# Performance work log

Hardware: AMD Instinct MI355X
Metric: run time of the kernel (lower is better)

## Reference

```python
import jax, jax.numpy as jnp
import numpy as np

N_NODES = 100000
N_EDGES = 1600000
F = 64
UNITS = 64


def setup_inputs() -> dict:
    key = jax.random.key(0)
    k = jax.random.split(key, 8)
    x = jax.random.normal(k[0], (N_NODES, F), dtype=jnp.float32)
    edge_index = jax.random.randint(k[1], (2, N_EDGES), 0, N_NODES, dtype=jnp.int32)
    edge_weight = jnp.ones((N_EDGES,), dtype=jnp.float32)
    # glorot-uniform-ish params
    def glorot(kk, shape):
        lim = np.sqrt(6.0 / (shape[0] + shape[1]))
        return jax.random.uniform(kk, shape, dtype=jnp.float32, minval=-lim, maxval=lim)
    mlp_kernel = glorot(k[2], (F, UNITS))
    mlp_bias = jnp.zeros((UNITS,), dtype=jnp.float32)
    neighs_kernel = glorot(k[3], (UNITS, UNITS))
    self_kernel = glorot(k[4], (F, UNITS))
    bias = jnp.zeros((2 * UNITS,), dtype=jnp.float32)
    return {"x": x, "edge_index": edge_index, "edge_weight": edge_weight,
            "mlp_kernel": mlp_kernel, "mlp_bias": mlp_bias,
            "neighs_kernel": neighs_kernel, "self_kernel": self_kernel, "bias": bias}


def reference(x, edge_index, edge_weight, mlp_kernel, mlp_bias, neighs_kernel, self_kernel, bias):
    num_nodes = x.shape[0]
    row, col = edge_index[0], edge_index[1]
    # gcn_mapper: neighbor message scaled by edge weight (original forces weights to 1)
    neighbor_x = x[col] * edge_weight[:, None]            # [E, F]
    h = jax.nn.relu(neighbor_x @ mlp_kernel + mlp_bias)   # [E, U]
    # unsorted_segment_mean over destination row (empty segments -> 0, matching TF)
    seg_sum = jax.ops.segment_sum(h, row, num_segments=num_nodes)              # [N, U]
    cnt = jax.ops.segment_sum(jnp.ones_like(row, dtype=h.dtype), row, num_segments=num_nodes)
    reduced_h = seg_sum / jnp.maximum(cnt, 1.0)[:, None]
    from_neighs = reduced_h @ neighs_kernel               # [N, U]
    from_x = x @ self_kernel                              # [N, U]
    out = jnp.concatenate([from_neighs, from_x], axis=1) + bias
    out = jax.nn.relu(out)                                # [N, 2U]
    return out
```

## Files before the change

### kernel.cpp

```cpp
#include <hip/hip_runtime.h>

#define MAXSLICE 12544
#define MAXSUB   800
#define NBH 32
#define IDXCAP 512

static __device__ __forceinline__ float relu_f(float v) { return fmaxf(v, 0.f); }

static __device__ __forceinline__ unsigned short f2bf(float f) {
  unsigned u = __float_as_uint(f);
  u += 0x7fffu + ((u >> 16) & 1u);
  return (unsigned short)(u >> 16);
}
static __device__ __forceinline__ float bf2f(unsigned short h) {
  return __uint_as_float(((unsigned)h) << 16);
}

__global__ __launch_bounds__(256) void k_node_dual_gemm(
    const float* __restrict__ x, const float* __restrict__ mk,
    const float* __restrict__ sk, const float* __restrict__ bias,
    unsigned short* __restrict__ xwh, float* __restrict__ out, int n_nodes,
    int* __restrict__ bcur0)
{
  __shared__ float s_mk[64][64];
  __shared__ float s_sk[64][64];
  __shared__ float s_xT[64][68];
  const int tid = threadIdx.x;
  if (bcur0 && blockIdx.x == 0 && tid < 8) bcur0[tid] = 0;
  for (int i = tid; i < 4096; i += 256) {
    s_mk[i >> 6][i & 63] = mk[i];
    s_sk[i >> 6][i & 63] = sk[i];
  }
  const int node0 = blockIdx.x * 64;
  for (int i = tid; i < 4096; i += 256) {
    int nl = i >> 6, f = i & 63;
    int n = node0 + nl;
    s_xT[f][nl] = (n < n_nodes) ? x[(size_t)n * 64 + f] : 0.f;
  }
  __syncthreads();
  const int g  = tid >> 4;
  const int ub = (tid & 15) * 4;
  float am[4][4] = {{0.f}};
  float as[4][4] = {{0.f}};
  for (int f = 0; f < 64; ++f) {
    float4 wm = *(const float4*)&s_mk[f][ub];
    float4 ws = *(const float4*)&s_sk[f][ub];
    float4 xv = *(const float4*)&s_xT[f][4 * g];
    const float xs[4] = {xv.x, xv.y, xv.z, xv.w};
#pragma unroll
    for (int j = 0; j < 4; ++j) {
      am[j][0] += xs[j] * wm.x; am[j][1] += xs[j] * wm.y;
      am[j][2] += xs[j] * wm.z; am[j][3] += xs[j] * wm.w;
      as[j][0] += xs[j] * ws.x; as[j][1] += xs[j] * ws.y;
      as[j][2] += xs[j] * ws.z; as[j][3] += xs[j] * ws.w;
    }
  }
  float4 bv = *(const float4*)&bias[64 + ub];
#pragma unroll
  for (int j = 0; j < 4; ++j) {
    int n = node0 + 4 * g + j;
    if (n >= n_nodes) break;
    ushort4 o1 = make_ushort4(f2bf(am[j][0]), f2bf(am[j][1]),
                              f2bf(am[j][2]), f2bf(am[j][3]));
    *(ushort4*)&xwh[(size_t)n * 64 + ub] = o1;
    *(float4*)&out[(size_t)n * 128 + 64 + ub] =
        make_float4(relu_f(as[j][0] + bv.x), relu_f(as[j][1] + bv.y),
                    relu_f(as[j][2] + bv.z), relu_f(as[j][3] + bv.w));
  }
}

__global__ __launch_bounds__(256) void k_count(
    const int* __restrict__ row, int* __restrict__ cnt, int n_edges)
{
  int e = blockIdx.x * 256 + threadIdx.x;
  if (e < n_edges) atomicAdd(&cnt[row[e]], 1);
}

__global__ __launch_bounds__(256) void k_build_sliced(
    const int* __restrict__ row, const int* __restrict__ col,
    const float* __restrict__ ew, int* __restrict__ off,
    int2* __restrict__ elist, int n_edges, int n_nodes)
{
  const int slice = blockIdx.x & 7;
  const int vb    = blockIdx.x >> 3;
  const int nvb   = gridDim.x >> 3;
  const int sliceN = (n_nodes + 7) >> 3;
  const int lo = slice * sliceN;
  const int hi = min(lo + sliceN, n_nodes);
  for (int e = vb * 256 + threadIdx.x; e < n_edges; e += nvb * 256) {
    int r = row[e];
    if (r >= lo && r < hi) {
      int pos = atomicAdd(&off[r], 1);
      elist[pos] = make_int2(col[e], __float_as_int(ew[e]));
    }
  }
}

__global__ __launch_bounds__(1024) void k_bsum(
    const int* __restrict__ cnt, int* __restrict__ bsum, int n)
{
  __shared__ int s[1024];
  int tid = threadIdx.x;
  int i = blockIdx.x * 1024 + tid;
  s[tid] = (i < n) ? cnt[i] : 0;
  __syncthreads();
  for (int d = 512; d > 0; d >>= 1) {
    if (tid < d) s[tid] += s[tid + d];
    __syncthreads();
  }
  if (tid == 0) bsum[blockIdx.x] = s[0];
}

__global__ __launch_bounds__(1024) void k_boffs(
    const int* __restrict__ cnt, const int* __restrict__ bsum,
    int* __restrict__ off, int n, int nb)
{
  __shared__ int s[1024];
  __shared__ int sp[128];
  int tid = threadIdx.x;
  if (tid < 128) {
    int acc = 0;
    for (int j = tid; j < blockIdx.x && j < nb; j += 128) acc += bsum[j];
    sp[tid] = acc;
  }
  int i = blockIdx.x * 1024 + tid;
  int v = (i < n) ? cnt[i] : 0;
  s[tid] = v;
  __syncthreads();
  for (int d = 64; d > 0; d >>= 1) {
    if (tid < d) sp[tid] += sp[tid + d];
    __syncthreads();
  }
  for (int d = 1; d < 1024; d <<= 1) {
    int t = (tid >= d) ? s[tid - d] : 0;
    __syncthreads();
    s[tid] += t;
    __syncthreads();
  }
  if (i < n) off[i] = s[tid] - v + sp[0];
}

__global__ __launch_bounds__(256) void k_bin(
    const int* __restrict__ row, const int* __restrict__ col,
    const float* __restrict__ ew,
    int* __restrict__ brow, int2* __restrict__ bpair,
    int* __restrict__ bcur, int n_edges, int sliceN, int cap)
{
  __shared__ int  s_wcnt[4][8];
  __shared__ int  s_tot[8];
  __shared__ int  s_toff[8];
  __shared__ int  s_gaddr[8];
  __shared__ int  s_rowst[1024];
  __shared__ int2 s_pairst[1024];
  const int tid  = threadIdx.x;
  const int wave = tid >> 6;
  const int lane = tid & 63;
  const unsigned usliceN = (unsigned)sliceN;
  const int stride = gridDim.x * 1024;
  for (int e0 = blockIdx.x * 1024; e0 < n_edges; e0 += stride) {
    const int e = e0 + 4 * tid;
    int   rr[4], cc[4];
    float ww[4];
    int   ss[4];
    if (e + 3 < n_edges) {
      int4 r4   = *(const int4*)&row[e];
      int4 c4   = *(const int4*)&col[e];
      float4 w4 = *(const float4*)&ew[e];
      rr[0] = r4.x; rr[1] = r4.y; rr[2] = r4.z; rr[3] = r4.w;
      cc[0] = c4.x; cc[1] = c4.y; cc[2] = c4.z; cc[3] = c4.w;
      ww[0] = w4.x; ww[1] = w4.y; ww[2] = w4.z; ww[3] = w4.w;
#pragma unroll
      for (int j = 0; j < 4; ++j) ss[j] = (int)((unsigned)rr[j] / usliceN);
    } else {
#pragma unroll
      for (int j = 0; j < 4; ++j) {
        int ej = e + j;
        bool v = ej < n_edges;
        rr[j] = v ? row[ej] : 0;
        cc[j] = v ? col[ej] : 0;
        ww[j] = v ? ew[ej]  : 0.f;
        ss[j] = v ? (int)((unsigned)rr[j] / usliceN) : -1;
      }
    }
#pragma unroll
    for (int b = 0; b < 8; ++b) {
      int c = 0;
#pragma unroll
      for (int j = 0; j < 4; ++j) c += __popcll(__ballot(ss[j] == b));
      if (lane == 0) s_wcnt[wave][b] = c;
    }
    __syncthreads();
    if (wave == 0 && lane < 8) {
      const int b = lane;
      int t0 = s_wcnt[0][b], t1 = s_wcnt[1][b], t2 = s_wcnt[2][b], t3 = s_wcnt[3][b];
      int tot = t0 + t1 + t2 + t3;
      s_tot[b] = tot;
      s_wcnt[0][b] = 0;
      s_wcnt[1][b] = t0;
      s_wcnt[2][b] = t0 + t1;
      s_wcnt[3][b] = t0 + t1 + t2;
      int gbase = tot ? atomicAdd(&bcur[b], tot) : 0;
      int pre = 0;
#pragma unroll
      for (int j2 = 0; j2 < 8; ++j2) pre += (j2 < b) ? s_tot[j2] : 0;
      s_toff[b]  = pre;
      s_gaddr[b] = b * cap + gbase - pre;
    }
    __syncthreads();
#pragma unroll
    for (int b = 0; b < 8; ++b) {
      const int sb = s_toff[b] + s_wcnt[wave][b];
      int off_local = 0;
#pragma unroll
      for (int j = 0; j < 4; ++j) {
        unsigned long long mm = __ballot(ss[j] == b);
        if (ss[j] == b) {
          int rank = __popcll(mm & ((1ull << lane) - 1ull));
          int slot = sb + off_local + rank;
          s_rowst[slot]  = rr[j];
          s_pairst[slot] = make_int2(cc[j], __float_as_int(ww[j]));
        }
        off_local += __popcll(mm);
      }
    }
    __syncthreads();
    const int total = s_toff[7] + s_tot[7];
    for (int i2 = tid; i2 < total; i2 += 256) {
      int b = 0;
#pragma unroll
      for (int j2 = 1; j2 < 8; ++j2) b += (i2 >= s_toff[j2]) ? 1 : 0;
      int a = s_gaddr[b] + i2;
      if (a < (b + 1) * cap) {
        brow[a]  = s_rowst[i2];
        bpair[a] = s_pairst[i2];
      }
    }
    __syncthreads();
  }
}

__global__ __launch_bounds__(256) void k_bin_idx(
    const int* __restrict__ row,
    int* __restrict__ brow, int* __restrict__ bidx,
    int* __restrict__ bcur, int n_edges, int sliceN, int cap)
{
  __shared__ int s_wcnt[4][8];
  __shared__ int s_tot[8];
  __shared__ int s_toff[8];
  __shared__ int s_gaddr[8];
  __shared__ int s_rowst[1024];
  __shared__ int s_idxst[1024];
  const int tid  = threadIdx.x;
  const int wave = tid >> 6;
  const int lane = tid & 63;
  const unsigned usliceN = (unsigned)sliceN;
  const int stride = gridDim.x * 1024;
  for (int e0 = blockIdx.x * 1024; e0 < n_edges; e0 += stride) {
    const int e = e0 + 4 * tid;
    int rr[4], ss[4];
    if (e + 3 < n_edges) {
      int4 r4 = *(const int4*)&row[e];
      rr[0] = r4.x; rr[1] = r4.y; rr[2] = r4.z; rr[3] = r4.w;
#pragma unroll
      for (int j = 0; j < 4; ++j) ss[j] = (int)((unsigned)rr[j] / usliceN);
    } else {
#pragma unroll
      for (int j = 0; j < 4; ++j) {
        int ej = e + j;
        bool v = ej < n_edges;
        rr[j] = v ? row[ej] : 0;
        ss[j] = v ? (int)((unsigned)rr[j] / usliceN) : -1;
      }
    }
#pragma unroll
    for (int b = 0; b < 8; ++b) {
      int c = 0;
#pragma unroll
      for (int j = 0; j < 4; ++j) c += __popcll(__ballot(ss[j] == b));
      if (lane == 0) s_wcnt[wave][b] = c;
    }
    __syncthreads();
    if (wave == 0 && lane < 8) {
      const int b = lane;
      int t0 = s_wcnt[0][b], t1 = s_wcnt[1][b], t2 = s_wcnt[2][b], t3 = s_wcnt[3][b];
      int tot = t0 + t1 + t2 + t3;
      s_tot[b] = tot;
      s_wcnt[0][b] = 0;
      s_wcnt[1][b] = t0;
      s_wcnt[2][b] = t0 + t1;
      s_wcnt[3][b] = t0 + t1 + t2;
      int gbase = tot ? atomicAdd(&bcur[b], tot) : 0;
      int pre = 0;
#pragma unroll
      for (int j2 = 0; j2 < 8; ++j2) pre += (j2 < b) ? s_tot[j2] : 0;
      s_toff[b]  = pre;
      s_gaddr[b] = b * cap + gbase - pre;
    }
    __syncthreads();
#pragma unroll
    for (int b = 0; b < 8; ++b) {
      const int sb = s_toff[b] + s_wcnt[wave][b];
      int off_local = 0;
#pragma unroll
      for (int j = 0; j < 4; ++j) {
        unsigned long long mm = __ballot(ss[j] == b);
        if (ss[j] == b) {
          int rank = __popcll(mm & ((1ull << lane) - 1ull));
          int slot = sb + off_local + rank;
          s_rowst[slot] = rr[j];
          s_idxst[slot] = e + j;
        }
        off_local += __popcll(mm);
      }
    }
    __syncthreads();
    const int total = s_toff[7] + s_tot[7];
    for (int i2 = tid; i2 < total; i2 += 256) {
      int b = 0;
#pragma unroll
      for (int j2 = 1; j2 < 8; ++j2) b += (i2 >= s_toff[j2]) ? 1 : 0;
      int a = s_gaddr[b] + i2;
      if (a < (b + 1) * cap) {
        brow[a] = s_rowst[i2];
        bidx[a] = s_idxst[i2];
      }
    }
    __syncthreads();
  }
}

__global__ __launch_bounds__(256) void k_hist(
    const int* __restrict__ brow, const int* __restrict__ bcur,
    int* __restrict__ hist, int cap, int chunk, int sliceN)
{
  __shared__ int h[MAXSLICE];
  const int s   = blockIdx.x & 7;
  const int blk = blockIdx.x >> 3;
  const int tid = threadIdx.x;
  for (int i = tid; i < MAXSLICE; i += 256) h[i] = 0;
  __syncthreads();
  const int n_s  = min(bcur[s], cap);
  const int lo_e = blk * chunk;
  const int hi_e = min(lo_e + chunk, n_s);
  const int base = s * cap;
  const int lo   = s * sliceN;
  for (int i = lo_e + tid; i < hi_e; i += 256) {
    atomicAdd(&h[brow[base + i] - lo], 1);
  }
  __syncthreads();
  int* hrow = hist + (size_t)(s * NBH + blk) * MAXSLICE;
  for (int i = tid; i < MAXSLICE / 4; i += 256) {
    ((int4*)hrow)[i] = ((const int4*)h)[i];
  }
}

__global__ __launch_bounds__(256) void k_colscan(
    int* __restrict__ hist, int* __restrict__ cnt, int sliceN, int n_nodes)
{
  const int s  = blockIdx.x & 7;
  const int cb = blockIdx.x >> 3;
  const int b0 = cb * 1024 + threadIdx.x * 4;
  if (b0 >= sliceN) return;
  int4 acc = make_int4(0, 0, 0, 0);
  int* hs = hist + (size_t)s * NBH * MAXSLICE;
#pragma unroll 4
  for (int blk = 0; blk < NBH; ++blk) {
    int4* p = (int4*)(hs + (size_t)blk * MAXSLICE + b0);
    int4 v = *p;
    *p = acc;
    acc.x += v.x; acc.y += v.y; acc.z += v.z; acc.w += v.w;
  }
  const int node = s * sliceN + b0;
  if (b0 + 3 < sliceN && node + 3 < n_nodes) {
    *(int4*)&cnt[node] = acc;
  } else {
    int a[4] = {acc.x, acc.y, acc.z, acc.w};
    for (int j = 0; j < 4; ++j)
      if (b0 + j < sliceN && node + j < n_nodes) cnt[node + j] = a[j];
  }
}

__global__ __launch_bounds__(256) void k_place(
    const int* __restrict__ brow, const int2* __restrict__ bpair,
    const int* __restrict__ bcur, const int* __restrict__ hist,
    const int* __restrict__ off, int2* __restrict__ elist,
    int cap, int chunk, int sliceN, int n_nodes)
{
  __shared__ int cur[MAXSLICE];
  const int s   = blockIdx.x & 7;
  const int blk = blockIdx.x >> 3;
  const int tid = threadIdx.x;
  const int lo  = s * sliceN;
  const int hi  = min(lo + sliceN, n_nodes);
  const int nb  = hi - lo;
  const int* hrow = hist + (size_t)(s * NBH + blk) * MAXSLICE;
  for (int i = tid; i < nb; i += 256) cur[i] = off[lo + i] + hrow[i];
  __syncthreads();
  const int n_s  = min(bcur[s], cap);
  const int lo_e = blk * chunk;
  const int hi_e = min(lo_e + chunk, n_s);
  const int base = s * cap;
  for (int i = lo_e + tid; i < hi_e; i += 256) {
    int r = brow[base + i] - lo;
    int p = atomicAdd(&cur[r], 1);
    elist[p] = bpair[base + i];
  }
}

__global__ __launch_bounds__(256) void k_fused_csr(
    const int* __restrict__ cnt, const int* __restrict__ off,
    const int2* __restrict__ elist, const unsigned short* __restrict__ xwh,
    const float* __restrict__ mb, const float* __restrict__ nk,
    const float* __restrict__ bias, float* __restrict__ out, int n_nodes,
    int starts)
{
  __shared__ float s_nk[64][64];
  __shared__ float s_rh[16][68];
  const int tid = threadIdx.x;
  for (int i = tid; i < 1024; i += 256) {
    *(float4*)&s_nk[0][4 * i] = *(const float4*)&nk[4 * i];
  }
  const int node_l = tid >> 4;
  const int q = tid & 15;
  const int n = blockIdx.x * 16 + node_l;
  float4 acc = make_float4(0.f, 0.f, 0.f, 0.f);
  if (n < n_nodes) {
    const float4 mbq = *(const float4*)&mb[4 * q];
    const int c = cnt[n];
    int i = off[n] - (starts ? 0 : c);
    const int end = i + c;
    for (; i + 8 <= end; i += 8) {
      int2 e[8];
#pragma unroll
      for (int j = 0; j < 8; ++j) e[j] = elist[i + j];
      ushort4 u[8];
#pragma unroll
      for (int j = 0; j < 8; ++j)
        u[j] = *(const ushort4*)&xwh[(size_t)e[j].x * 64 + 4 * q];
#pragma unroll
      for (int j = 0; j < 8; ++j) {
        float w = __int_as_float(e[j].y);
        acc.x += relu_f(w * bf2f(u[j].x) + mbq.x);
        acc.y += relu_f(w * bf2f(u[j].y) + mbq.y);
        acc.z += relu_f(w * bf2f(u[j].z) + mbq.z);
        acc.w += relu_f(w * bf2f(u[j].w) + mbq.w);
      }
    }
    if (i + 4 <= end) {
      int2 e[4];
#pragma unroll
      for (int j = 0; j < 4; ++j) e[j] = elist[i + j];
      ushort4 u[4];
#pragma unroll
      for (int j = 0; j < 4; ++j)
        u[j] = *(const ushort4*)&xwh[(size_t)e[j].x * 64 + 4 * q];
#pragma unroll
      for (int j = 0; j < 4; ++j) {
        float w = __int_as_float(e[j].y);
        acc.x += relu_f(w * bf2f(u[j].x) + mbq.x);
        acc.y += relu_f(w * bf2f(u[j].y) + mbq.y);
        acc.z += relu_f(w * bf2f(u[j].z) + mbq.z);
        acc.w += relu_f(w * bf2f(u[j].w) + mbq.w);
      }
      i += 4;
    }
    for (; i < end; ++i) {
      int2 e0 = elist[i];
      ushort4 u0 = *(const ushort4*)&xwh[(size_t)e0.x * 64 + 4 * q];
      float w0 = __int_as_float(e0.y);
      acc.x += relu_f(w0 * bf2f(u0.x) + mbq.x);
      acc.y += relu_f(w0 * bf2f(u0.y) + mbq.y);
      acc.z += relu_f(w0 * bf2f(u0.z) + mbq.z);
      acc.w += relu_f(w0 * bf2f(u0.w) + mbq.w);
    }
    const float inv = 1.0f / fmaxf((float)c, 1.0f);
    acc.x *= inv; acc.y *= inv; acc.z *= inv; acc.w *= inv;
  }
  *(float4*)&s_rh[node_l][4 * q] = acc;
  __syncthreads();
  float4 o = make_float4(0.f, 0.f, 0.f, 0.f);
  for (int f = 0; f < 64; ++f) {
    float rv = s_rh[node_l][f];
    float4 wv = *(const float4*)&s_nk[f][4 * q];
    o.x += rv * wv.x; o.y += rv * wv.y; o.z += rv * wv.z; o.w += rv * wv.w;
  }
  if (n < n_nodes) {
    float4 bv = *(const float4*)&bias[4 * q];
    *(float4*)&out[(size_t)n * 128 + 4 * q] =
        make_float4(relu_f(o.x + bv.x), relu_f(o.y + bv.y),
                    relu_f(o.z + bv.z), relu_f(o.w + bv.w));
  }
}

__global__ __launch_bounds__(256) void k_hist16(
    const int* __restrict__ brow, const int* __restrict__ bcur,
    int* __restrict__ hist, int cap, int chunk, int sliceN)
{
  __shared__ int h[MAXSUB];
  const int s   = blockIdx.x & 7;
  const int blk = blockIdx.x >> 3;
  const int tid = threadIdx.x;
  const int nsub = (sliceN + 15) >> 4;
  for (int i = tid; i < nsub; i += 256) h[i] = 0;
  __syncthreads();
  const int n_s  = min(bcur[s], cap);
  const int lo_e = blk * chunk;
  const int hi_e = min(lo_e + chunk, n_s);
  const int base = s * cap;
  const int lo   = s * sliceN;
  for (int i = lo_e + tid; i < hi_e; i += 256) {
    atomicAdd(&h[(brow[base + i] - lo) >> 4], 1);
  }
  __syncthreads();
  int* hrow = hist + (size_t)(s * NBH + blk) * MAXSUB;
  for (int i = tid; i < nsub; i += 256) hrow[i] = h[i];
}

__global__ __launch_bounds__(1024) void k_colscan16(
    int* __restrict__ hist, const int* __restrict__ bcur,
    int* __restrict__ off_sub, int cap, int sliceN)
{
  __shared__ int s_t[1024];
  const int s = blockIdx.x;
  const int tid = threadIdx.x;
  const int nsub = (sliceN + 15) >> 4;
  int acc = 0;
  if (tid < nsub) {
    int* hs = hist + (size_t)s * NBH * MAXSUB;
    for (int blk = 0; blk < NBH; ++blk) {
      int* p = hs + (size_t)blk * MAXSUB + tid;
      int v = *p;
      *p = acc;
      acc += v;
    }
  }
  s_t[tid] = (tid < nsub) ? acc : 0;
  __syncthreads();
  for (int d = 1; d < 1024; d <<= 1) {
    int t = (tid >= d) ? s_t[tid - d] : 0;
    __syncthreads();
    s_t[tid] += t;
    __syncthreads();
  }
  int base = 0;
  for (int b = 0; b < s; ++b) base += min(bcur[b], cap);
  int excl = (tid == 0) ? 0 : s_t[tid - 1];
  if (tid < nsub) off_sub[s * nsub + tid] = base + excl;
  if (s == 7 && tid == 1023) off_sub[8 * nsub] = base + s_t[1023];
}

__global__ __launch_bounds__(256) void k_place16_idx(
    const int* __restrict__ brow, const int* __restrict__ bidx,
    const int* __restrict__ col, const float* __restrict__ ew,
    const int* __restrict__ bcur, const int* __restrict__ hist,
    const int* __restrict__ off_sub, int2* __restrict__ elist,
    int cap, int chunk, int sliceN)
{
  __shared__ int cur[MAXSUB];
  const int s   = blockIdx.x & 7;
  const int blk = blockIdx.x >> 3;
  const int tid = threadIdx.x;
  const int nsub = (sliceN + 15) >> 4;
  const int* hrow = hist + (size_t)(s * NBH + blk) * MAXSUB;
  for (int i = tid; i < nsub; i += 256) cur[i] = off_sub[s * nsub + i] + hrow[i];
  __syncthreads();
  const int n_s  = min(bcur[s], cap);
  const int lo_e = blk * chunk;
  const int hi_e = min(lo_e + chunk, n_s);
  const int base = s * cap;
  const int lo   = s * sliceN;
  for (int i = lo_e + tid; i < hi_e; i += 256) {
    int rloc = brow[base + i] - lo;
    int idx  = bidx[base + i];
    int p = atomicAdd(&cur[rloc >> 4], 1);
    elist[p] = make_int2(col[idx] | ((rloc & 15) << 27), __float_as_int(ew[idx]));
  }
}

__global__ __launch_bounds__(256) void k_fused_sub(
    const int* __restrict__ osub, const int2* __restrict__ elist,
    const unsigned short* __restrict__ xwh, const float* __restrict__ mb,
    const float* __restrict__ nk, const float* __restrict__ bias,
    float* __restrict__ out, int n_nodes, int sliceN)
{
  __shared__ float s_nk[64][64];
  __shared__ float s_rh[16][68];
  __shared__ int s_h[16];
  __shared__ int s_pre[17];
  __shared__ int s_cur[16];
  __shared__ unsigned short s_idx[IDXCAP];
  const int tid = threadIdx.x;
  for (int i = tid; i < 1024; i += 256) {
    *(float4*)&s_nk[0][4 * i] = *(const float4*)&nk[4 * i];
  }
  const int s   = blockIdx.x & 7;
  const int sub = blockIdx.x >> 3;
  const int nsub = (sliceN + 15) >> 4;
  const int e0 = osub[s * nsub + sub];
  const int e1 = osub[s * nsub + sub + 1];
  const int g = tid >> 4;
  const int q = tid & 15;
  const float4 mbq = *(const float4*)&mb[4 * q];
  float4 acc = make_float4(0.f, 0.f, 0.f, 0.f);
  int cnt_g = 0;
  for (int c0 = e0; c0 < e1; c0 += IDXCAP) {
    const int m = min(IDXCAP, e1 - c0);
    if (tid < 16) s_h[tid] = 0;
    __syncthreads();
    for (int i = tid; i < m; i += 256) {
      atomicAdd(&s_h[((unsigned)elist[c0 + i].x) >> 27], 1);
    }
    __syncthreads();
    if (tid == 0) {
      int a = 0;
#pragma unroll
      for (int b = 0; b < 16; ++b) { s_pre[b] = a; s_cur[b] = a; a += s_h[b]; }
      s_pre[16] = a;
    }
    __syncthreads();
    for (int i = tid; i < m; i += 256) {
      int rl = ((unsigned)elist[c0 + i].x) >> 27;
      int p = atomicAdd(&s_cur[rl], 1);
      s_idx[p] = (unsigned short)i;
    }
    __syncthreads();
    const int st = s_pre[g];
    const int cN = s_h[g];
    cnt_g += cN;
    int k = 0;
    for (; k + 8 <= cN; k += 8) {
      int2 e[8];
#pragma unroll
      for (int j = 0; j < 8; ++j) e[j] = elist[c0 + s_idx[st + k + j]];
      ushort4 u[8];
#pragma unroll
      for (int j = 0; j < 8; ++j)
        u[j] = *(const ushort4*)&xwh[(size_t)(e[j].x & 0x07FFFFFF) * 64 + 4 * q];
#pragma unroll
      for (int j = 0; j < 8; ++j) {
        float w = __int_as_float(e[j].y);
        acc.x += relu_f(w * bf2f(u[j].x) + mbq.x);
        acc.y += relu_f(w * bf2f(u[j].y) + mbq.y);
        acc.z += relu_f(w * bf2f(u[j].z) + mbq.z);
        acc.w += relu_f(w * bf2f(u[j].w) + mbq.w);
      }
    }
    if (k + 4 <= cN) {
      int2 e[4];
#pragma unroll
      for (int j = 0; j < 4; ++j) e[j] = elist[c0 + s_idx[st + k + j]];
      ushort4 u[4];
#pragma unroll
      for (int j = 0; j < 4; ++j)
        u[j] = *(const ushort4*)&xwh[(size_t)(e[j].x & 0x07FFFFFF) * 64 + 4 * q];
#pragma unroll
      for (int j = 0; j < 4; ++j) {
        float w = __int_as_float(e[j].y);
        acc.x += relu_f(w * bf2f(u[j].x) + mbq.x);
        acc.y += relu_f(w * bf2f(u[j].y) + mbq.y);
        acc.z += relu_f(w * bf2f(u[j].z) + mbq.z);
        acc.w += relu_f(w * bf2f(u[j].w) + mbq.w);
      }
      k += 4;
    }
    for (; k < cN; ++k) {
      int2 ev = elist[c0 + s_idx[st + k]];
      ushort4 u0 = *(const ushort4*)&xwh[(size_t)(ev.x & 0x07FFFFFF) * 64 + 4 * q];
      float w = __int_as_float(ev.y);
      acc.x += relu_f(w * bf2f(u0.x) + mbq.x);
      acc.y += relu_f(w * bf2f(u0.y) + mbq.y);
      acc.z += relu_f(w * bf2f(u0.z) + mbq.z);
      acc.w += relu_f(w * bf2f(u0.w) + mbq.w);
    }
    __syncthreads();
  }
  const float inv = 1.0f / fmaxf((float)cnt_g, 1.0f);
  acc.x *= inv; acc.y *= inv; acc.z *= inv; acc.w *= inv;
  *(float4*)&s_rh[g][4 * q] = acc;
  __syncthreads();
  float4 o = make_float4(0.f, 0.f, 0.f, 0.f);
  for (int f = 0; f < 64; ++f) {
    float rv = s_rh[g][f];
    float4 wv = *(const float4*)&s_nk[f][4 * q];
    o.x += rv * wv.x; o.y += rv * wv.y; o.z += rv * wv.z; o.w += rv * wv.w;
  }
  const int loc = sub * 16 + g;
  const int n = s * sliceN + loc;
  if (loc < sliceN && n < n_nodes) {
    float4 bv = *(const float4*)&bias[4 * q];
    *(float4*)&out[(size_t)n * 128 + 4 * q] =
        make_float4(relu_f(o.x + bv.x), relu_f(o.y + bv.y),
                    relu_f(o.z + bv.z), relu_f(o.w + bv.w));
  }
}

extern "C" void kernel_launch(void* const* d_in, const int* in_sizes, int n_in,
                              void* d_out, int out_size, void* d_ws, size_t ws_size,
                              hipStream_t stream) {
  const float* x    = (const float*)d_in[0];
  const int*   ei   = (const int*)d_in[1];
  const float* ew   = (const float*)d_in[2];
  const float* mk   = (const float*)d_in[3];
  const float* mb   = (const float*)d_in[4];
  const float* nk   = (const float*)d_in[5];
  const float* sk   = (const float*)d_in[6];
  const float* bias = (const float*)d_in[7];
  float* out = (float*)d_out;

  const int n_nodes = in_sizes[0] / 64;
  const int n_edges = in_sizes[2];
  const int* row = ei;
  const int* col = ei + n_edges;

  unsigned short* xwh = (unsigned short*)d_ws;
  int*  cnt  = (int*)(xwh + (size_t)n_nodes * 64);
  int*  bcur = cnt + n_nodes;
  int*  off  = bcur + 8;
  int*  bsum = off + n_nodes;
  int*  osub = bsum + 128;
  size_t ebytes = ((size_t)((char*)(osub + 8 * MAXSUB + 8) - (char*)d_ws) + 7) & ~(size_t)7;
  int2* elist = (int2*)((char*)d_ws + ebytes);
  const int cap = (n_edges >> 3) + 8192;
  int*  brow  = (int*)(elist + n_edges);
  size_t pboff = (((size_t)((char*)(brow + (size_t)8 * cap) - (char*)d_ws)) + 7) & ~(size_t)7;
  int2* bpair = (int2*)((char*)d_ws + pboff);
  int*  bidx  = (int*)bpair;
  size_t need_b = (size_t)((char*)(bpair + (size_t)8 * cap) - (char*)d_ws);
  size_t hoff = (need_b + 15) & ~(size_t)15;
  int*  hist  = (int*)((char*)d_ws + hoff);
  size_t need_a = hoff + (size_t)8 * NBH * MAXSLICE * sizeof(int);

  const int nb_scan = (n_nodes + 1023) / 1024;
  const int sliceN = (n_nodes + 7) >> 3;
  const int nsub = (sliceN + 15) >> 4;
  const int nbn = (n_nodes + 63) / 64;
  const int nbf = (n_nodes + 15) / 16;
  const int chunk = (cap + NBH - 1) / NBH;

  const bool fitsA = (ws_size >= need_a) && (sliceN <= MAXSLICE);
  const bool subOK = fitsA && (nsub <= MAXSUB) && (n_nodes >= 16) &&
                     (n_nodes < (1 << 27)) && ((size_t)8 * cap >= (size_t)n_edges);

  if (subOK) {
    k_node_dual_gemm<<<nbn, 256, 0, stream>>>(x, mk, sk, bias, xwh, out,
                                              n_nodes, bcur);
    int nbb = (n_edges + 1023) / 1024;
    if (nbb > 2048) nbb = 2048;
    k_bin_idx<<<nbb, 256, 0, stream>>>(row, brow, bidx, bcur,
                                       n_edges, sliceN, cap);
    k_hist16<<<8 * NBH, 256, 0, stream>>>(brow, bcur, hist, cap, chunk, sliceN);
    k_colscan16<<<8, 1024, 0, stream>>>(hist, bcur, osub, cap, sliceN);
    k_place16_idx<<<8 * NBH, 256, 0, stream>>>(brow, bidx, col, ew, bcur, hist,
                                               osub, elist, cap, chunk, sliceN);
    k_fused_sub<<<8 * nsub, 256, 0, stream>>>(osub, elist, xwh, mb, nk, bias,
                                              out, n_nodes, sliceN);
  } else if (fitsA) {
    hipMemsetAsync(bcur, 0, 8 * sizeof(int), stream);
    k_node_dual_gemm<<<nbn, 256, 0, stream>>>(x, mk, sk, bias, xwh, out,
                                              n_nodes, nullptr);
    int nbb = (n_edges + 1023) / 1024;
    if (nbb > 2048) nbb = 2048;
    k_bin<<<nbb, 256, 0, stream>>>(row, col, ew, brow, bpair, bcur,
                                   n_edges, sliceN, cap);
    k_hist<<<8 * NBH, 256, 0, stream>>>(brow, bcur, hist, cap, chunk, sliceN);
    const int ncb = (sliceN + 1023) / 1024;
    k_colscan<<<8 * ncb, 256, 0, stream>>>(hist, cnt, sliceN, n_nodes);
    k_bsum<<<nb_scan, 1024, 0, stream>>>(cnt, bsum, n_nodes);
    k_boffs<<<nb_scan, 1024, 0, stream>>>(cnt, bsum, off, n_nodes, nb_scan);
    k_place<<<8 * NBH, 256, 0, stream>>>(brow, bpair, bcur, hist, off,
                                         elist, cap, chunk, sliceN, n_nodes);
    k_fused_csr<<<nbf, 256, 0, stream>>>(cnt, off, elist, xwh, mb, nk,
                                         bias, out, n_nodes, 1);
  } else {
    hipMemsetAsync(cnt, 0, (size_t)n_nodes * sizeof(int), stream);
    k_node_dual_gemm<<<nbn, 256, 0, stream>>>(x, mk, sk, bias, xwh, out,
                                              n_nodes, nullptr);
    const int nbe = (n_edges + 255) / 256;
    k_count<<<nbe, 256, 0, stream>>>(row, cnt, n_edges);
    k_bsum<<<nb_scan, 1024, 0, stream>>>(cnt, bsum, n_nodes);
    k_boffs<<<nb_scan, 1024, 0, stream>>>(cnt, bsum, off, n_nodes, nb_scan);
    k_build_sliced<<<1024, 256, 0, stream>>>(row, col, ew, off, elist,
                                             n_edges, n_nodes);
    k_fused_csr<<<nbf, 256, 0, stream>>>(cnt, off, elist, xwh, mb, nk,
                                         bias, out, n_nodes, 0);
  }
}
```

Measured before the change: 270.3 us.

## Fuse node GEMM with edge binning and pack col/local-row into binned payload

Merges the node dual-GEMM and the edge binning pass into one launch: the first nbn blocks run the GEMM and the rest bin edges, with shared memory overlaid through a union. Binning now also reads col and edge weight and writes a packed (col | local row << 17) word plus the weight. This removes the later random gathers of col[idx] and ew[idx] in the placement kernel and drops one kernel launch. The cost is a memset launch for the bin counters, more bytes read during binning, and a tighter node-count limit (< 2^17) for the fast path.

```diff
diff --git a/kernel.cpp b/kernel.cpp
--- a/kernel.cpp
+++ b/kernel.cpp
@@ -16,17 +16,168 @@
   return __uint_as_float(((unsigned)h) << 16);
 }
 
+__global__ __launch_bounds__(256) void k_gemm_bin(
+    const float* __restrict__ x, const float* __restrict__ mk,
+    const float* __restrict__ sk, const float* __restrict__ bias,
+    unsigned short* __restrict__ xwh, float* __restrict__ out, int n_nodes,
+    const int* __restrict__ row, const int* __restrict__ col,
+    const float* __restrict__ ew,
+    int* __restrict__ bpk, float* __restrict__ bew, int* __restrict__ bcur,
+    int n_edges, int sliceN, int cap, int nbn)
+{
+  __shared__ union U {
+    struct { float mks[64][64]; float sks[64][64]; float xT[64][68]; } g;
+    struct { int wcnt[4][8]; int tot[8]; int toff[8]; int gaddr[8];
+             int pk[1024]; float ww[1024]; } b;
+  } u;
+  const int tid = threadIdx.x;
+
+  if (blockIdx.x < nbn) {
+    for (int i = tid; i < 4096; i += 256) {
+      u.g.mks[i >> 6][i & 63] = mk[i];
+      u.g.sks[i >> 6][i & 63] = sk[i];
+    }
+    const int node0 = blockIdx.x * 64;
+    for (int i = tid; i < 4096; i += 256) {
+      int nl = i >> 6, f = i & 63;
+      int n = node0 + nl;
+      u.g.xT[f][nl] = (n < n_nodes) ? x[(size_t)n * 64 + f] : 0.f;
+    }
+    __syncthreads();
+    const int g  = tid >> 4;
+    const int ub = (tid & 15) * 4;
+    float am[4][4] = {{0.f}};
+    float as[4][4] = {{0.f}};
+    for (int f = 0; f < 64; ++f) {
+      float4 wm = *(const float4*)&u.g.mks[f][ub];
+      float4 ws = *(const float4*)&u.g.sks[f][ub];
+      float4 xv = *(const float4*)&u.g.xT[f][4 * g];
+      const float xs[4] = {xv.x, xv.y, xv.z, xv.w};
+#pragma unroll
+      for (int j = 0; j < 4; ++j) {
+        am[j][0] += xs[j] * wm.x; am[j][1] += xs[j] * wm.y;
+        am[j][2] += xs[j] * wm.z; am[j][3] += xs[j] * wm.w;
+        as[j][0] += xs[j] * ws.x; as[j][1] += xs[j] * ws.y;
+        as[j][2] += xs[j] * ws.z; as[j][3] += xs[j] * ws.w;
+      }
+    }
+    float4 bv = *(const float4*)&bias[64 + ub];
+#pragma unroll
+    for (int j = 0; j < 4; ++j) {
+      int n = node0 + 4 * g + j;
+      if (n >= n_nodes) break;
+      ushort4 o1 = make_ushort4(f2bf(am[j][0]), f2bf(am[j][1]),
+                                f2bf(am[j][2]), f2bf(am[j][3]));
+      *(ushort4*)&xwh[(size_t)n * 64 + ub] = o1;
+      *(float4*)&out[(size_t)n * 128 + 64 + ub] =
+          make_float4(relu_f(as[j][0] + bv.x), relu_f(as[j][1] + bv.y),
+                      relu_f(as[j][2] + bv.z), relu_f(as[j][3] + bv.w));
+    }
+    return;
+  }
+
+  const int vbid = blockIdx.x - nbn;
+  const int nvb  = gridDim.x - nbn;
+  const int wave = tid >> 6;
+  const int lane = tid & 63;
+  const unsigned usliceN = (unsigned)sliceN;
+  const int stride = nvb * 1024;
+  for (int e0 = vbid * 1024; e0 < n_edges; e0 += stride) {
+    const int e = e0 + 4 * tid;
+    int   pp[4];
+    float ww[4];
+    int   ss[4];
+    if (e + 3 < n_edges) {
+      int4 r4   = *(const int4*)&row[e];
+      int4 c4   = *(const int4*)&col[e];
+      float4 w4 = *(const float4*)&ew[e];
+      int rr[4] = {r4.x, r4.y, r4.z, r4.w};
+      int cc[4] = {c4.x, c4.y, c4.z, c4.w};
+      ww[0] = w4.x; ww[1] = w4.y; ww[2] = w4.z; ww[3] = w4.w;
+#pragma unroll
+      for (int j = 0; j < 4; ++j) {
+        ss[j] = (int)((unsigned)rr[j] / usliceN);
+        pp[j] = cc[j] | ((rr[j] - ss[j] * sliceN) << 17);
+      }
+    } else {
+#pragma unroll
+      for (int j = 0; j < 4; ++j) {
+        int ej = e + j;
+        bool v = ej < n_edges;
+        int r = v ? row[ej] : 0;
+        int c = v ? col[ej] : 0;
+        ww[j] = v ? ew[ej] : 0.f;
+        ss[j] = v ? (int)((unsigned)r / usliceN) : -1;
+        pp[j] = v ? (c | ((r - ss[j] * sliceN) << 17)) : 0;
+      }
+    }
+#pragma unroll
+    for (int b = 0; b < 8; ++b) {
+      int c = 0;
+#pragma unroll
+      for (int j = 0; j < 4; ++j) c += __popcll(__ballot(ss[j] == b));
+      if (lane == 0) u.b.wcnt[wave][b] = c;
+    }
+    __syncthreads();
+    if (wave == 0 && lane < 8) {
+      const int b = lane;
+      int t0 = u.b.wcnt[0][b], t1 = u.b.wcnt[1][b];
+      int t2 = u.b.wcnt[2][b], t3 = u.b.wcnt[3][b];
+      int tot = t0 + t1 + t2 + t3;
+      u.b.tot[b] = tot;
+      u.b.wcnt[0][b] = 0;
+      u.b.wcnt[1][b] = t0;
+      u.b.wcnt[2][b] = t0 + t1;
+      u.b.wcnt[3][b] = t0 + t1 + t2;
+      int gbase = tot ? atomicAdd(&bcur[b], tot) : 0;
+      int pre = 0;
+#pragma unroll
+      for (int j2 = 0; j2 < 8; ++j2) pre += (j2 < b) ? u.b.tot[j2] : 0;
+      u.b.toff[b]  = pre;
+      u.b.gaddr[b] = b * cap + gbase - pre;
+    }
+    __syncthreads();
+#pragma unroll
+    for (int b = 0; b < 8; ++b) {
+      const int sb = u.b.toff[b] + u.b.wcnt[wave][b];
+      int off_local = 0;
+#pragma unroll
+      for (int j = 0; j < 4; ++j) {
+        unsigned long long mm = __ballot(ss[j] == b);
+        if (ss[j] == b) {
+          int rank = __popcll(mm & ((1ull << lane) - 1ull));
+          int slot = sb + off_local + rank;
+          u.b.pk[slot] = pp[j];
+          u.b.ww[slot] = ww[j];
+        }
+        off_local += __popcll(mm);
+      }
+    }
+    __syncthreads();
+    const int total = u.b.toff[7] + u.b.tot[7];
+    for (int i2 = tid; i2 < total; i2 += 256) {
+      int b = 0;
+#pragma unroll
+      for (int j2 = 1; j2 < 8; ++j2) b += (i2 >= u.b.toff[j2]) ? 1 : 0;
+      int a = u.b.gaddr[b] + i2;
+      if (a < (b + 1) * cap) {
+        bpk[a] = u.b.pk[i2];
+        bew[a] = u.b.ww[i2];
+      }
+    }
+    __syncthreads();
+  }
+}
+
 __global__ __launch_bounds__(256) void k_node_dual_gemm(
     const float* __restrict__ x, const float* __restrict__ mk,
     const float* __restrict__ sk, const float* __restrict__ bias,
-    unsigned short* __restrict__ xwh, float* __restrict__ out, int n_nodes,
-    int* __restrict__ bcur0)
+    unsigned short* __restrict__ xwh, float* __restrict__ out, int n_nodes)
 {
   __shared__ float s_mk[64][64];
   __shared__ float s_sk[64][64];
   __shared__ float s_xT[64][68];
   const int tid = threadIdx.x;
-  if (bcur0 && blockIdx.x == 0 && tid < 8) bcur0[tid] = 0;
   for (int i = tid; i < 4096; i += 256) {
     s_mk[i >> 6][i & 63] = mk[i];
     s_sk[i >> 6][i & 63] = sk[i];
@@ -239,96 +390,6 @@
   }
 }
 
-__global__ __launch_bounds__(256) void k_bin_idx(
-    const int* __restrict__ row,
-    int* __restrict__ brow, int* __restrict__ bidx,
-    int* __restrict__ bcur, int n_edges, int sliceN, int cap)
-{
-  __shared__ int s_wcnt[4][8];
-  __shared__ int s_tot[8];
-  __shared__ int s_toff[8];
-  __shared__ int s_gaddr[8];
-  __shared__ int s_rowst[1024];
-  __shared__ int s_idxst[1024];
-  const int tid  = threadIdx.x;
-  const int wave = tid >> 6;
-  const int lane = tid & 63;
-  const unsigned usliceN = (unsigned)sliceN;
-  const int stride = gridDim.x * 1024;
-  for (int e0 = blockIdx.x * 1024; e0 < n_edges; e0 += stride) {
-    const int e = e0 + 4 * tid;
-    int rr[4], ss[4];
-    if (e + 3 < n_edges) {
-      int4 r4 = *(const int4*)&row[e];
-      rr[0] = r4.x; rr[1] = r4.y; rr[2] = r4.z; rr[3] = r4.w;
-#pragma unroll
-      for (int j = 0; j < 4; ++j) ss[j] = (int)((unsigned)rr[j] / usliceN);
-    } else {
-#pragma unroll
-      for (int j = 0; j < 4; ++j) {
-        int ej = e + j;
-        bool v = ej < n_edges;
-        rr[j] = v ? row[ej] : 0;
-        ss[j] = v ? (int)((unsigned)rr[j] / usliceN) : -1;
-      }
-    }
-#pragma unroll
-    for (int b = 0; b < 8; ++b) {
-      int c = 0;
-#pragma unroll
-      for (int j = 0; j < 4; ++j) c += __popcll(__ballot(ss[j] == b));
-      if (lane == 0) s_wcnt[wave][b] = c;
-    }
-    __syncthreads();
-    if (wave == 0 && lane < 8) {
-      const int b = lane;
-      int t0 = s_wcnt[0][b], t1 = s_wcnt[1][b], t2 = s_wcnt[2][b], t3 = s_wcnt[3][b];
-      int tot = t0 + t1 + t2 + t3;
-      s_tot[b] = tot;
-      s_wcnt[0][b] = 0;
-      s_wcnt[1][b] = t0;
-      s_wcnt[2][b] = t0 + t1;
-      s_wcnt[3][b] = t0 + t1 + t2;
-      int gbase = tot ? atomicAdd(&bcur[b], tot) : 0;
-      int pre = 0;
-#pragma unroll
-      for (int j2 = 0; j2 < 8; ++j2) pre += (j2 < b) ? s_tot[j2] : 0;
-      s_toff[b]  = pre;
-      s_gaddr[b] = b * cap + gbase - pre;
-    }
-    __syncthreads();
-#pragma unroll
-    for (int b = 0; b < 8; ++b) {
-      const int sb = s_toff[b] + s_wcnt[wave][b];
-      int off_local = 0;
-#pragma unroll
-      for (int j = 0; j < 4; ++j) {
-        unsigned long long mm = __ballot(ss[j] == b);
-        if (ss[j] == b) {
-          int rank = __popcll(mm & ((1ull << lane) - 1ull));
-          int slot = sb + off_local + rank;
-          s_rowst[slot] = rr[j];
-          s_idxst[slot] = e + j;
-        }
-        off_local += __popcll(mm);
-      }
-    }
-    __syncthreads();
-    const int total = s_toff[7] + s_tot[7];
-    for (int i2 = tid; i2 < total; i2 += 256) {
-      int b = 0;
-#pragma unroll
-      for (int j2 = 1; j2 < 8; ++j2) b += (i2 >= s_toff[j2]) ? 1 : 0;
-      int a = s_gaddr[b] + i2;
-      if (a < (b + 1) * cap) {
-        brow[a] = s_rowst[i2];
-        bidx[a] = s_idxst[i2];
-      }
-    }
-    __syncthreads();
-  }
-}
-
 __global__ __launch_bounds__(256) void k_hist(
     const int* __restrict__ brow, const int* __restrict__ bcur,
     int* __restrict__ hist, int cap, int chunk, int sliceN)
@@ -492,8 +553,8 @@
   }
 }
 
-__global__ __launch_bounds__(256) void k_hist16(
-    const int* __restrict__ brow, const int* __restrict__ bcur,
+__global__ __launch_bounds__(256) void k_hist16_pk(
+    const int* __restrict__ bpk, const int* __restrict__ bcur,
     int* __restrict__ hist, int cap, int chunk, int sliceN)
 {
   __shared__ int h[MAXSUB];
@@ -507,9 +568,8 @@
   const int lo_e = blk * chunk;
   const int hi_e = min(lo_e + chunk, n_s);
   const int base = s * cap;
-  const int lo   = s * sliceN;
   for (int i = lo_e + tid; i < hi_e; i += 256) {
-    atomicAdd(&h[(brow[base + i] - lo) >> 4], 1);
+    atomicAdd(&h[((unsigned)bpk[base + i]) >> 21], 1);
   }
   __syncthreads();
   int* hrow = hist + (size_t)(s * NBH + blk) * MAXSUB;
@@ -549,9 +609,8 @@
   if (s == 7 && tid == 1023) off_sub[8 * nsub] = base + s_t[1023];
 }
 
-__global__ __launch_bounds__(256) void k_place16_idx(
-    const int* __restrict__ brow, const int* __restrict__ bidx,
-    const int* __restrict__ col, const float* __restrict__ ew,
+__global__ __launch_bounds__(256) void k_place16_pk(
+    const int* __restrict__ bpk, const float* __restrict__ bew,
     const int* __restrict__ bcur, const int* __restrict__ hist,
     const int* __restrict__ off_sub, int2* __restrict__ elist,
     int cap, int chunk, int sliceN)
@@ -568,12 +627,12 @@
   const int lo_e = blk * chunk;
   const int hi_e = min(lo_e + chunk, n_s);
   const int base = s * cap;
-  const int lo   = s * sliceN;
   for (int i = lo_e + tid; i < hi_e; i += 256) {
-    int rloc = brow[base + i] - lo;
-    int idx  = bidx[base + i];
-    int p = atomicAdd(&cur[rloc >> 4], 1);
-    elist[p] = make_int2(col[idx] | ((rloc & 15) << 27), __float_as_int(ew[idx]));
+    unsigned pk = (unsigned)bpk[base + i];
+    float w = bew[base + i];
+    int p = atomicAdd(&cur[pk >> 21], 1);
+    elist[p] = make_int2((int)((pk & 0x1FFFFu) | (((pk >> 17) & 15u) << 27)),
+                         __float_as_int(w));
   }
 }
 
@@ -724,7 +783,8 @@
   int*  brow  = (int*)(elist + n_edges);
   size_t pboff = (((size_t)((char*)(brow + (size_t)8 * cap) - (char*)d_ws)) + 7) & ~(size_t)7;
   int2* bpair = (int2*)((char*)d_ws + pboff);
-  int*  bidx  = (int*)bpair;
+  int*   bpk  = brow;
+  float* bew  = (float*)bpair;
   size_t need_b = (size_t)((char*)(bpair + (size_t)8 * cap) - (char*)d_ws);
   size_t hoff = (need_b + 15) & ~(size_t)15;
   int*  hist  = (int*)((char*)d_ws + hoff);
@@ -739,25 +799,26 @@
 
   const bool fitsA = (ws_size >= need_a) && (sliceN <= MAXSLICE);
   const bool subOK = fitsA && (nsub <= MAXSUB) && (n_nodes >= 16) &&
-                     (n_nodes < (1 << 27)) && ((size_t)8 * cap >= (size_t)n_edges);
+                     (n_nodes < (1 << 17)) &&
+                     ((size_t)8 * cap >= (size_t)n_edges);
 
   if (subOK) {
-    k_node_dual_gemm<<<nbn, 256, 0, stream>>>(x, mk, sk, bias, xwh, out,
-                                              n_nodes, bcur);
+    hipMemsetAsync(bcur, 0, 8 * sizeof(int), stream);
     int nbb = (n_edges + 1023) / 1024;
     if (nbb > 2048) nbb = 2048;
-    k_bin_idx<<<nbb, 256, 0, stream>>>(row, brow, bidx, bcur,
-                                       n_edges, sliceN, cap);
-    k_hist16<<<8 * NBH, 256, 0, stream>>>(brow, bcur, hist, cap, chunk, sliceN);
+    if (nbb < 1) nbb = 1;
+    k_gemm_bin<<<nbn + nbb, 256, 0, stream>>>(x, mk, sk, bias, xwh, out, n_nodes,
+                                              row, col, ew, bpk, bew, bcur,
+                                              n_edges, sliceN, cap, nbn);
+    k_hist16_pk<<<8 * NBH, 256, 0, stream>>>(bpk, bcur, hist, cap, chunk, sliceN);
     k_colscan16<<<8, 1024, 0, stream>>>(hist, bcur, osub, cap, sliceN);
-    k_place16_idx<<<8 * NBH, 256, 0, stream>>>(brow, bidx, col, ew, bcur, hist,
-                                               osub, elist, cap, chunk, sliceN);
+    k_place16_pk<<<8 * NBH, 256, 0, stream>>>(bpk, bew, bcur, hist, osub,
+                                              elist, cap, chunk, sliceN);
     k_fused_sub<<<8 * nsub, 256, 0, stream>>>(osub, elist, xwh, mb, nk, bias,
                                               out, n_nodes, sliceN);
   } else if (fitsA) {
     hipMemsetAsync(bcur, 0, 8 * sizeof(int), stream);
-    k_node_dual_gemm<<<nbn, 256, 0, stream>>>(x, mk, sk, bias, xwh, out,
-                                              n_nodes, nullptr);
+    k_node_dual_gemm<<<nbn, 256, 0, stream>>>(x, mk, sk, bias, xwh, out, n_nodes);
     int nbb = (n_edges + 1023) / 1024;
     if (nbb > 2048) nbb = 2048;
     k_bin<<<nbb, 256, 0, stream>>>(row, col, ew, brow, bpair, bcur,
@@ -773,8 +834,7 @@
                                          bias, out, n_nodes, 1);
   } else {
     hipMemsetAsync(cnt, 0, (size_t)n_nodes * sizeof(int), stream);
-    k_node_dual_gemm<<<nbn, 256, 0, stream>>>(x, mk, sk, bias, xwh, out,
-                                              n_nodes, nullptr);
+    k_node_dual_gemm<<<nbn, 256, 0, stream>>>(x, mk, sk, bias, xwh, out, n_nodes);
     const int nbe = (n_edges + 255) / 256;
     k_count<<<nbe, 256, 0, stream>>>(row, cnt, n_edges);
     k_bsum<<<nb_scan, 1024, 0, stream>>>(cnt, bsum, n_nodes);
```

Result: faster. 235.7 us, median of 2 (-12.8%).
